# Kernel optimization log

Measured on AMD Instinct MI355X. Metric: run time of the kernel, lower is better.

The kernel has to match this reference:

```python
import jax, jax.numpy as jnp
import numpy as np

N, E, F_IN, F_EDGE, HID, OUT = 100000, 1600000, 128, 8, 128, 2
BN_EPS = 1e-5


def setup_inputs() -> dict:
    key = jax.random.key(0)
    ks = jax.random.split(key, 16)
    rn = lambda k, shape, s=0.05: jax.random.normal(k, shape, jnp.float32) * s
    return {
        "x": jax.random.normal(ks[0], (N, F_IN), jnp.float32),
        "edge_attr": jax.random.uniform(ks[1], (E, F_EDGE), dtype=jnp.float32),
        "edge_index": jax.random.randint(ks[2], (2, E), 0, N, jnp.int32),
        # edge MLP: Linear(F_EDGE, HID) -> ReLU -> Linear(HID, 1) -> Sigmoid
        "ew1_w": rn(ks[3], (F_EDGE, HID)), "ew1_b": jnp.zeros((HID,), jnp.float32),
        "ew2_w": rn(ks[4], (HID, 1)), "ew2_b": jnp.zeros((1,), jnp.float32),
        # SAGEConv layers: lin_l (on aggregated neighbors, with bias) + lin_r (root)
        "w1_l": rn(ks[5], (F_IN, HID)), "b1_l": jnp.zeros((HID,), jnp.float32), "w1_r": rn(ks[6], (F_IN, HID)),
        "w2_l": rn(ks[7], (HID, HID)), "b2_l": jnp.zeros((HID,), jnp.float32), "w2_r": rn(ks[8], (HID, HID)),
        "w3_l": rn(ks[9], (HID, OUT)), "b3_l": jnp.zeros((OUT,), jnp.float32), "w3_r": rn(ks[10], (HID, OUT)),
        # BatchNorm1d (eval mode: running stats)
        "bn1_g": jnp.ones((HID,), jnp.float32), "bn1_b": jnp.zeros((HID,), jnp.float32),
        "bn1_m": rn(ks[11], (HID,), 0.01), "bn1_v": jnp.ones((HID,), jnp.float32),
        "bn2_g": jnp.ones((HID,), jnp.float32), "bn2_b": jnp.zeros((HID,), jnp.float32),
        "bn2_m": rn(ks[12], (HID,), 0.01), "bn2_v": jnp.ones((HID,), jnp.float32),
    }


def _sage(x, src, dst, ew, w_l, b_l, w_r):
    # PyG SAGEConv(aggr='mean'): msg = x[src] * edge_weight, mean over incoming edges at dst
    msg = x[src] * ew[:, None]                                  # [E, F]
    s = jax.ops.segment_sum(msg, dst, num_segments=N)           # [N, F]
    deg = jax.ops.segment_sum(jnp.ones((src.shape[0],), x.dtype), dst, num_segments=N)
    agg = s / jnp.maximum(deg, 1.0)[:, None]
    return agg @ w_l + b_l + x @ w_r


def _bn_eval(h, g, b, m, v):
    return (h - m) * jax.lax.rsqrt(v + BN_EPS) * g + b


def reference(x, edge_attr, edge_index,
              ew1_w, ew1_b, ew2_w, ew2_b,
              w1_l, b1_l, w1_r, w2_l, b2_l, w2_r, w3_l, b3_l, w3_r,
              bn1_g, bn1_b, bn1_m, bn1_v, bn2_g, bn2_b, bn2_m, bn2_v):
    src, dst = edge_index[0], edge_index[1]
    # per-edge scalar weight from small MLP
    ew = jax.nn.sigmoid(jax.nn.relu(edge_attr @ ew1_w + ew1_b) @ ew2_w + ew2_b).reshape(-1)
    h = _sage(x, src, dst, ew, w1_l, b1_l, w1_r)
    h = jax.nn.relu(_bn_eval(h, bn1_g, bn1_b, bn1_m, bn1_v))    # dropout no-op in eval
    h = _sage(h, src, dst, ew, w2_l, b2_l, w2_r)
    h = jax.nn.relu(_bn_eval(h, bn2_g, bn2_b, bn2_m, bn2_v))
    return _sage(h, src, dst, ew, w3_l, b3_l, w3_r)
```

## Files before the change

kernel.cpp:

```cpp
#include <hip/hip_runtime.h>
#include <math.h>

#define N_NODES 100000
#define N_EDGES 1600000
#define F_INF   128
#define HIDF    128

typedef __attribute__((ext_vector_type(8)))  short short8;
typedef __attribute__((ext_vector_type(16))) float floatx16;

__device__ __forceinline__ unsigned short f2bf(float f) {
    unsigned u = __float_as_uint(f);
    return (unsigned short)((u + 0x7FFFu + ((u >> 16) & 1u)) >> 16);
}

__global__ __launch_bounds__(256) void k_edge_mlp(
        const float* __restrict__ ea,
        const float* __restrict__ w1, const float* __restrict__ b1,
        const float* __restrict__ w2, const float* __restrict__ b2,
        float* __restrict__ ew) {
    const int lane = threadIdx.x & 63;
    const int cl   = lane & 31;
    const int half = lane >> 5;
    const int wid  = blockIdx.x * (blockDim.x >> 6) + (threadIdx.x >> 6);
    const int nw   = gridDim.x * (blockDim.x >> 6);

    short8 bw[4];
    float  w2c[4];
#pragma unroll
    for (int cb = 0; cb < 4; ++cb) {
        const int n = cb * 32 + cl;
        short8 b;
        if (half == 0) {
#pragma unroll
            for (int j = 0; j < 8; ++j) b[j] = (short)f2bf(w1[j * 128 + n]);
        } else {
            b[0] = (short)f2bf(b1[n]);
#pragma unroll
            for (int j = 1; j < 8; ++j) b[j] = 0;
        }
        bw[cb] = b;
        w2c[cb] = w2[n];
    }
    short8 Abias;
    Abias[0] = (short)0x3F80;
#pragma unroll
    for (int j = 1; j < 8; ++j) Abias[j] = 0;

    floatx16 czero;
#pragma unroll
    for (int r = 0; r < 16; ++r) czero[r] = 0.f;

    const float bias2 = b2[0];

    for (int e0 = wid * 32; e0 < N_EDGES; e0 += nw * 32) {
        short8 Ah;
        if (half == 0) {
            const float4 a0 = *(const float4*)(ea + (size_t)(e0 + cl) * 8);
            const float4 a1 = *(const float4*)(ea + (size_t)(e0 + cl) * 8 + 4);
            Ah[0] = (short)f2bf(a0.x); Ah[1] = (short)f2bf(a0.y);
            Ah[2] = (short)f2bf(a0.z); Ah[3] = (short)f2bf(a0.w);
            Ah[4] = (short)f2bf(a1.x); Ah[5] = (short)f2bf(a1.y);
            Ah[6] = (short)f2bf(a1.z); Ah[7] = (short)f2bf(a1.w);
        } else {
            Ah = Abias;
        }

        float z[16];
#pragma unroll
        for (int r = 0; r < 16; ++r) z[r] = 0.f;

#pragma unroll
        for (int cb = 0; cb < 4; ++cb) {
            floatx16 acc = __builtin_amdgcn_mfma_f32_32x32x16_bf16(Ah, bw[cb], czero, 0, 0, 0);
#pragma unroll
            for (int r = 0; r < 16; ++r)
                z[r] = fmaf(fmaxf(acc[r], 0.f), w2c[cb], z[r]);
        }

#pragma unroll
        for (int m = 1; m <= 16; m <<= 1) {
#pragma unroll
            for (int r = 0; r < 16; ++r) z[r] += __shfl_xor(z[r], m, 64);
        }

        float zz = z[0];
#pragma unroll
        for (int r = 1; r < 16; ++r) zz = (cl == r) ? z[r] : zz;
        if (cl < 16) {
            const int row = (cl & 3) + 8 * (cl >> 2) + 4 * half;
            ew[e0 + row] = 1.f / (1.f + __expf(-(zz + bias2)));
        }
    }
}

__global__ void k_deg(const int* __restrict__ dst, int* __restrict__ deg,
                      unsigned char* __restrict__ rank) {
    int e = blockIdx.x * 256 + threadIdx.x;
    if (e < N_EDGES) rank[e] = (unsigned char)atomicAdd(&deg[dst[e]], 1);
}

__global__ void k_scan1(const int* __restrict__ deg, int* __restrict__ incl,
                        int* __restrict__ bsum) {
    __shared__ int sm[1024];
    const int tid = threadIdx.x;
    const int gi  = blockIdx.x * 1024 + tid;
    int v = (gi < N_NODES) ? deg[gi] : 0;
    sm[tid] = v;
    __syncthreads();
    for (int off = 1; off < 1024; off <<= 1) {
        int t = (tid >= off) ? sm[tid - off] : 0;
        __syncthreads();
        sm[tid] += t;
        __syncthreads();
    }
    if (gi < N_NODES) incl[gi] = sm[tid];
    if (tid == 1023) bsum[blockIdx.x] = sm[1023];
}

__global__ void k_scan2(const int* __restrict__ bsum, int* __restrict__ boff, int nb) {
    __shared__ int sm[128];
    const int tid = threadIdx.x;
    int v = (tid < nb) ? bsum[tid] : 0;
    sm[tid] = v;
    __syncthreads();
    for (int off = 1; off < 128; off <<= 1) {
        int t = (tid >= off) ? sm[tid - off] : 0;
        __syncthreads();
        sm[tid] += t;
        __syncthreads();
    }
    boff[tid] = sm[tid] - v;
}

__global__ void k_scan3(const int* __restrict__ incl, const int* __restrict__ boff,
                        int* __restrict__ rowptr) {
    int i = blockIdx.x * 256 + threadIdx.x;
    if (i < N_NODES) rowptr[i + 1] = boff[i >> 10] + incl[i];
    if (i == 0) rowptr[0] = 0;
}

__global__ void k_fill(const int* __restrict__ src, const int* __restrict__ dst,
                       const float* __restrict__ ew, const int* __restrict__ rowptr,
                       const unsigned char* __restrict__ rank,
                       unsigned* __restrict__ cw) {
    int e = blockIdx.x * 256 + threadIdx.x;
    if (e < N_EDGES) {
        int d   = dst[e];
        int pos = rowptr[d] + (int)rank[e];
        unsigned wb = (unsigned)f2bf(ew[e]) & 0x7FFFu;
        cw[pos] = ((unsigned)src[e] << 15) | wb;
    }
}

__global__ void k_cast(const float* __restrict__ x, unsigned short* __restrict__ xb) {
    const int i = (blockIdx.x * 256 + threadIdx.x) * 4;
    const float4 v = *(const float4*)(x + i);
    ushort4 o;
    o.x = f2bf(v.x); o.y = f2bf(v.y); o.z = f2bf(v.z); o.w = f2bf(v.w);
    *(ushort4*)(xb + i) = o;
}

__global__ __launch_bounds__(256) void k_agg16(
        const unsigned short* __restrict__ xb, const int* __restrict__ rowptr,
        const unsigned* __restrict__ cw, float* __restrict__ aggout) {
    const int lane = threadIdx.x & 63;
    const int half = lane >> 5;
    const int cl   = lane & 31;
    const int node = blockIdx.x * (blockDim.x >> 6) + (threadIdx.x >> 6);
    if (node >= N_NODES) return;
    const int s = rowptr[node], e = rowptr[node + 1];
    float a0 = 0.f, a1 = 0.f, a2 = 0.f, a3 = 0.f;

    for (int j0 = s; j0 < e; j0 += 8) {
        int ss[4]; float ww[4];
#pragma unroll
        for (int u = 0; u < 4; ++u) {
            const int j  = j0 + 2 * u + half;
            const int jc = min(j, e - 1);
            const unsigned p = cw[jc];
            ss[u] = (int)(p >> 15);
            ww[u] = (j < e) ? __uint_as_float((p & 0x7FFFu) << 16) : 0.f;
        }
        uint2 g[4];
#pragma unroll
        for (int u = 0; u < 4; ++u)
            g[u] = *(const uint2*)(xb + (size_t)ss[u] * 128 + cl * 4);
#pragma unroll
        for (int u = 0; u < 4; ++u) {
            const float f0 = __uint_as_float(g[u].x << 16);
            const float f1 = __uint_as_float(g[u].x & 0xFFFF0000u);
            const float f2 = __uint_as_float(g[u].y << 16);
            const float f3 = __uint_as_float(g[u].y & 0xFFFF0000u);
            a0 = fmaf(ww[u], f0, a0);
            a1 = fmaf(ww[u], f1, a1);
            a2 = fmaf(ww[u], f2, a2);
            a3 = fmaf(ww[u], f3, a3);
        }
    }
    a0 += __shfl_xor(a0, 32, 64);
    a1 += __shfl_xor(a1, 32, 64);
    a2 += __shfl_xor(a2, 32, 64);
    a3 += __shfl_xor(a3, 32, 64);
    if (half == 0) {
        const float inv = 1.f / fmaxf((float)(e - s), 1.f);
        float4 r;
        r.x = a0 * inv; r.y = a1 * inv; r.z = a2 * inv; r.w = a3 * inv;
        *(float4*)(aggout + (size_t)node * 128 + cl * 4) = r;
    }
}

__global__ void k_wpack(const float* __restrict__ Wl, const float* __restrict__ Wr,
                        short* __restrict__ Whi, short* __restrict__ Wlo) {
    int idx = blockIdx.x * 256 + threadIdx.x;
    int j  = idx & 7;
    int L  = (idx >> 3) & 63;
    int cb = (idx >> 9) & 3;
    int kb = (idx >> 11);
    int k  = kb * 16 + (L >> 5) * 8 + j;
    int n  = cb * 32 + (L & 31);
    float a = (k < 128) ? Wl[k * 128 + n] : Wr[(k - 128) * 128 + n];
    unsigned short hb = f2bf(a);
    float hf = __uint_as_float((unsigned)hb << 16);
    Whi[idx] = (short)hb;
    Wlo[idx] = (short)f2bf(a - hf);
}

__global__ __launch_bounds__(256) void k_gemm_mfma(
    const float* __restrict__ Aagg, const float* __restrict__ Ax,
    const short* __restrict__ Whi, const short* __restrict__ Wlo,
    const float* __restrict__ bl,
    const float* __restrict__ bng, const float* __restrict__ bnb,
    const float* __restrict__ bnm, const float* __restrict__ bnv,
    float* __restrict__ out, unsigned short* __restrict__ out16) {
    const int tid  = threadIdx.x;
    const int lane = tid & 63;
    const int w    = tid >> 6;
    const int row0 = blockIdx.x * 128 + w * 32;
    const int rrow = lane & 31;
    const int kq   = lane >> 5;
    const int arow = min(row0 + rrow, N_NODES - 1);

    floatx16 acc[4];
#pragma unroll
    for (int cb = 0; cb < 4; ++cb)
#pragma unroll
        for (int r = 0; r < 16; ++r) acc[cb][r] = 0.f;

    const float* Abase0 = Aagg + (size_t)arow * 128 + kq * 8;
    const float* Abase1 = Ax   + (size_t)arow * 128 + kq * 8;

#pragma unroll 2
    for (int kb = 0; kb < 16; ++kb) {
        const float* ap = ((kb < 8) ? Abase0 : Abase1) + (kb & 7) * 16;
        const float4 a0 = *(const float4*)(ap);
        const float4 a1 = *(const float4*)(ap + 4);
        const float av[8] = {a0.x, a0.y, a0.z, a0.w, a1.x, a1.y, a1.z, a1.w};
        short8 Ah, Al;
#pragma unroll
        for (int j = 0; j < 8; ++j) {
            unsigned short hb = f2bf(av[j]);
            float hf = __uint_as_float((unsigned)hb << 16);
            Ah[j] = (short)hb;
            Al[j] = (short)f2bf(av[j] - hf);
        }
#pragma unroll
        for (int cb = 0; cb < 4; ++cb) {
            const size_t wo = ((size_t)(kb * 4 + cb) * 64 + lane) * 8;
            const short8 wh = *(const short8*)(Whi + wo);
            const short8 wl = *(const short8*)(Wlo + wo);
            acc[cb] = __builtin_amdgcn_mfma_f32_32x32x16_bf16(Ah, wh, acc[cb], 0, 0, 0);
            acc[cb] = __builtin_amdgcn_mfma_f32_32x32x16_bf16(Al, wh, acc[cb], 0, 0, 0);
            acc[cb] = __builtin_amdgcn_mfma_f32_32x32x16_bf16(Ah, wl, acc[cb], 0, 0, 0);
        }
    }

#pragma unroll
    for (int cb = 0; cb < 4; ++cb) {
        const int c = cb * 32 + (lane & 31);
        const float s = bng[c] * rsqrtf(bnv[c] + 1e-5f);
        const float t = (bl[c] - bnm[c]) * s + bnb[c];
#pragma unroll
        for (int r = 0; r < 16; ++r) {
            const int row = row0 + (r & 3) + 8 * (r >> 2) + 4 * kq;
            if (row < N_NODES) {
                const float v = fmaxf(fmaf(acc[cb][r], s, t), 0.f);
                out[(size_t)row * 128 + c] = v;
                if (out16) out16[(size_t)row * 128 + c] = f2bf(v);
            }
        }
    }
}

__global__ void k_lin3(const float* __restrict__ h, const float* __restrict__ w3l,
                       const float* __restrict__ w3r, float* __restrict__ t4) {
    const int lane = threadIdx.x & 63;
    const int node = blockIdx.x * (blockDim.x >> 6) + (threadIdx.x >> 6);
    if (node >= N_NODES) return;
    float h0 = h[(size_t)node * 128 + lane];
    float h1 = h[(size_t)node * 128 + 64 + lane];
    float2 wl0 = *(const float2*)(w3l + lane * 2);
    float2 wl1 = *(const float2*)(w3l + (64 + lane) * 2);
    float2 wr0 = *(const float2*)(w3r + lane * 2);
    float2 wr1 = *(const float2*)(w3r + (64 + lane) * 2);
    float p0 = h0 * wl0.x + h1 * wl1.x;
    float p1 = h0 * wl0.y + h1 * wl1.y;
    float p2 = h0 * wr0.x + h1 * wr1.x;
    float p3 = h0 * wr0.y + h1 * wr1.y;
#pragma unroll
    for (int m = 1; m < 64; m <<= 1) {
        p0 += __shfl_xor(p0, m, 64);
        p1 += __shfl_xor(p1, m, 64);
        p2 += __shfl_xor(p2, m, 64);
        p3 += __shfl_xor(p3, m, 64);
    }
    if (lane == 0) {
        float4 o; o.x = p0; o.y = p1; o.z = p2; o.w = p3;
        *(float4*)(t4 + (size_t)node * 4) = o;
    }
}

__global__ void k_out(const float* __restrict__ t4, const int* __restrict__ rowptr,
                      const unsigned* __restrict__ cw,
                      const float* __restrict__ b3, float* __restrict__ out) {
    const int lane = threadIdx.x & 63;
    const int node = blockIdx.x * (blockDim.x >> 6) + (threadIdx.x >> 6);
    if (node >= N_NODES) return;
    const int s = rowptr[node], e = rowptr[node + 1];
    float a0 = 0.f, a1 = 0.f;
    for (int j = s + lane; j < e; j += 64) {
        const unsigned p = cw[j];
        const int   sr = (int)(p >> 15);
        const float w  = __uint_as_float((p & 0x7FFFu) << 16);
        float2 t = *(const float2*)(t4 + (size_t)sr * 4);
        a0 += w * t.x; a1 += w * t.y;
    }
#pragma unroll
    for (int m = 1; m < 64; m <<= 1) {
        a0 += __shfl_xor(a0, m, 64);
        a1 += __shfl_xor(a1, m, 64);
    }
    if (lane == 0) {
        float inv = 1.f / fmaxf((float)(e - s), 1.f);
        float2 o;
        o.x = a0 * inv + b3[0] + t4[(size_t)node * 4 + 2];
        o.y = a1 * inv + b3[1] + t4[(size_t)node * 4 + 3];
        *(float2*)(out + (size_t)node * 2) = o;
    }
}

extern "C" void kernel_launch(void* const* d_in, const int* in_sizes, int n_in,
                              void* d_out, int out_size, void* d_ws, size_t ws_size,
                              hipStream_t stream) {
    const float* x    = (const float*)d_in[0];
    const float* ea   = (const float*)d_in[1];
    const int*   ei   = (const int*)d_in[2];
    const float* ew1w = (const float*)d_in[3];
    const float* ew1b = (const float*)d_in[4];
    const float* ew2w = (const float*)d_in[5];
    const float* ew2b = (const float*)d_in[6];
    const float* w1l  = (const float*)d_in[7];
    const float* b1l  = (const float*)d_in[8];
    const float* w1r  = (const float*)d_in[9];
    const float* w2l  = (const float*)d_in[10];
    const float* b2l  = (const float*)d_in[11];
    const float* w2r  = (const float*)d_in[12];
    const float* w3l  = (const float*)d_in[13];
    const float* b3l  = (const float*)d_in[14];
    const float* w3r  = (const float*)d_in[15];
    const float* bn1g = (const float*)d_in[16];
    const float* bn1b = (const float*)d_in[17];
    const float* bn1m = (const float*)d_in[18];
    const float* bn1v = (const float*)d_in[19];
    const float* bn2g = (const float*)d_in[20];
    const float* bn2b = (const float*)d_in[21];
    const float* bn2m = (const float*)d_in[22];
    const float* bn2v = (const float*)d_in[23];

    const int* src = ei;
    const int* dst = ei + N_EDGES;
    float* out = (float*)d_out;

    size_t off = 0;
    auto carve = [&](size_t bytes) -> void* {
        void* p = (char*)d_ws + off;
        off += (bytes + 255) & ~(size_t)255;
        return p;
    };
    float* ew     = (float*)carve((size_t)N_EDGES * 4);
    unsigned* cw  = (unsigned*)carve((size_t)N_EDGES * 4);
    unsigned char* rank = (unsigned char*)carve((size_t)N_EDGES);
    int*   rowptr = (int*)carve((size_t)(N_NODES + 1) * 4);
    int*   deg    = (int*)carve((size_t)N_NODES * 4);
    int*   bsum   = (int*)carve(128 * 4);
    int*   boff   = (int*)carve(128 * 4);
    int*   incl   = (int*)carve((size_t)N_NODES * 4);
    float* agg    = (float*)carve((size_t)N_NODES * 128 * 4);
    float* hA     = (float*)carve((size_t)N_NODES * 128 * 4);
    float* hB     = (float*)carve((size_t)N_NODES * 128 * 4);
    float* t4     = (float*)carve((size_t)N_NODES * 4 * 4);
    short* W1hi   = (short*)carve(32768 * 2);
    short* W1lo   = (short*)carve(32768 * 2);
    short* W2hi   = (short*)carve(32768 * 2);
    short* W2lo   = (short*)carve(32768 * 2);
    unsigned short* xb   = (unsigned short*)carve((size_t)N_NODES * 128 * 2);
    unsigned short* hA16 = (unsigned short*)carve((size_t)N_NODES * 128 * 2);
    (void)ws_size; (void)n_in; (void)in_sizes; (void)out_size;

    hipMemsetAsync(deg, 0, (size_t)N_NODES * 4, stream);

    const int EB = (N_EDGES + 255) / 256;
    const int NB_SCAN = (N_NODES + 1023) / 1024;
    const int NWB = (N_NODES + 3) / 4;
    const int GB = (N_NODES + 127) / 128;
    const int CB = (N_NODES * 128 / 4 + 255) / 256;

    k_deg<<<EB, 256, 0, stream>>>(dst, deg, rank);
    k_cast<<<CB, 256, 0, stream>>>(x, xb);
    k_edge_mlp<<<2048, 256, 0, stream>>>(ea, ew1w, ew1b, ew2w, ew2b, ew);
    k_wpack<<<128, 256, 0, stream>>>(w1l, w1r, W1hi, W1lo);
    k_wpack<<<128, 256, 0, stream>>>(w2l, w2r, W2hi, W2lo);
    k_scan1<<<NB_SCAN, 1024, 0, stream>>>(deg, incl, bsum);
    k_scan2<<<1, 128, 0, stream>>>(bsum, boff, NB_SCAN);
    k_scan3<<<(N_NODES + 255) / 256, 256, 0, stream>>>(incl, boff, rowptr);
    k_fill<<<EB, 256, 0, stream>>>(src, dst, ew, rowptr, rank, cw);

    k_agg16<<<NWB, 256, 0, stream>>>(xb, rowptr, cw, agg);
    k_gemm_mfma<<<GB, 256, 0, stream>>>(agg, x, W1hi, W1lo, b1l,
                                        bn1g, bn1b, bn1m, bn1v, hA, hA16);
    k_agg16<<<NWB, 256, 0, stream>>>(hA16, rowptr, cw, agg);
    k_gemm_mfma<<<GB, 256, 0, stream>>>(agg, hA, W2hi, W2lo, b2l,
                                        bn2g, bn2b, bn2m, bn2v, hB, nullptr);
    k_lin3<<<NWB, 256, 0, stream>>>(hB, w3l, w3r, t4);
    k_out<<<NWB, 256, 0, stream>>>(t4, rowptr, cw, b3l, out);
}
```

Baseline: 591.5 us.

## Fuse neighbor aggregation with MFMA GEMM and layer-3 projection per 32-node tile

```diff
diff --git a/kernel.cpp b/kernel.cpp
--- a/kernel.cpp
+++ b/kernel.cpp
@@ -12,6 +12,9 @@
 __device__ __forceinline__ unsigned short f2bf(float f) {
     unsigned u = __float_as_uint(f);
     return (unsigned short)((u + 0x7FFFu + ((u >> 16) & 1u)) >> 16);
+}
+__device__ __forceinline__ float bf2f(unsigned short h) {
+    return __uint_as_float((unsigned)h << 16);
 }
 
 __global__ __launch_bounds__(256) void k_edge_mlp(
@@ -94,10 +97,19 @@
     }
 }
 
-__global__ void k_deg(const int* __restrict__ dst, int* __restrict__ deg,
-                      unsigned char* __restrict__ rank) {
-    int e = blockIdx.x * 256 + threadIdx.x;
-    if (e < N_EDGES) rank[e] = (unsigned char)atomicAdd(&deg[dst[e]], 1);
+__global__ void k_cast_deg(const float* __restrict__ x, unsigned short* __restrict__ xb,
+                           const int* __restrict__ dst, int* __restrict__ deg,
+                           unsigned char* __restrict__ rank) {
+    const int gid = blockIdx.x * 256 + threadIdx.x;
+    const int i = gid * 4;
+    const float4 v = *(const float4*)(x + i);
+    ushort4 o;
+    o.x = f2bf(v.x); o.y = f2bf(v.y); o.z = f2bf(v.z); o.w = f2bf(v.w);
+    *(ushort4*)(xb + i) = o;
+    if ((gid & 1) == 0) {
+        const int e = gid >> 1;
+        rank[e] = (unsigned char)atomicAdd(&deg[dst[e]], 1);
+    }
 }
 
 __global__ void k_scan1(const int* __restrict__ deg, int* __restrict__ incl,
@@ -150,63 +162,6 @@
         int pos = rowptr[d] + (int)rank[e];
         unsigned wb = (unsigned)f2bf(ew[e]) & 0x7FFFu;
         cw[pos] = ((unsigned)src[e] << 15) | wb;
-    }
-}
-
-__global__ void k_cast(const float* __restrict__ x, unsigned short* __restrict__ xb) {
-    const int i = (blockIdx.x * 256 + threadIdx.x) * 4;
-    const float4 v = *(const float4*)(x + i);
-    ushort4 o;
-    o.x = f2bf(v.x); o.y = f2bf(v.y); o.z = f2bf(v.z); o.w = f2bf(v.w);
-    *(ushort4*)(xb + i) = o;
-}
-
-__global__ __launch_bounds__(256) void k_agg16(
-        const unsigned short* __restrict__ xb, const int* __restrict__ rowptr,
-        const unsigned* __restrict__ cw, float* __restrict__ aggout) {
-    const int lane = threadIdx.x & 63;
-    const int half = lane >> 5;
-    const int cl   = lane & 31;
-    const int node = blockIdx.x * (blockDim.x >> 6) + (threadIdx.x >> 6);
-    if (node >= N_NODES) return;
-    const int s = rowptr[node], e = rowptr[node + 1];
-    float a0 = 0.f, a1 = 0.f, a2 = 0.f, a3 = 0.f;
-
-    for (int j0 = s; j0 < e; j0 += 8) {
-        int ss[4]; float ww[4];
-#pragma unroll
-        for (int u = 0; u < 4; ++u) {
-            const int j  = j0 + 2 * u + half;
-            const int jc = min(j, e - 1);
-            const unsigned p = cw[jc];
-            ss[u] = (int)(p >> 15);
-            ww[u] = (j < e) ? __uint_as_float((p & 0x7FFFu) << 16) : 0.f;
-        }
-        uint2 g[4];
-#pragma unroll
-        for (int u = 0; u < 4; ++u)
-            g[u] = *(const uint2*)(xb + (size_t)ss[u] * 128 + cl * 4);
-#pragma unroll
-        for (int u = 0; u < 4; ++u) {
-            const float f0 = __uint_as_float(g[u].x << 16);
-            const float f1 = __uint_as_float(g[u].x & 0xFFFF0000u);
-            const float f2 = __uint_as_float(g[u].y << 16);
-            const float f3 = __uint_as_float(g[u].y & 0xFFFF0000u);
-            a0 = fmaf(ww[u], f0, a0);
-            a1 = fmaf(ww[u], f1, a1);
-            a2 = fmaf(ww[u], f2, a2);
-            a3 = fmaf(ww[u], f3, a3);
-        }
-    }
-    a0 += __shfl_xor(a0, 32, 64);
-    a1 += __shfl_xor(a1, 32, 64);
-    a2 += __shfl_xor(a2, 32, 64);
-    a3 += __shfl_xor(a3, 32, 64);
-    if (half == 0) {
-        const float inv = 1.f / fmaxf((float)(e - s), 1.f);
-        float4 r;
-        r.x = a0 * inv; r.y = a1 * inv; r.z = a2 * inv; r.w = a3 * inv;
-        *(float4*)(aggout + (size_t)node * 128 + cl * 4) = r;
     }
 }
 
@@ -226,44 +181,92 @@
     Wlo[idx] = (short)f2bf(a - hf);
 }
 
-__global__ __launch_bounds__(256) void k_gemm_mfma(
-    const float* __restrict__ Aagg, const float* __restrict__ Ax,
-    const short* __restrict__ Whi, const short* __restrict__ Wlo,
-    const float* __restrict__ bl,
-    const float* __restrict__ bng, const float* __restrict__ bnb,
-    const float* __restrict__ bnm, const float* __restrict__ bnv,
-    float* __restrict__ out, unsigned short* __restrict__ out16) {
-    const int tid  = threadIdx.x;
-    const int lane = tid & 63;
-    const int w    = tid >> 6;
-    const int row0 = blockIdx.x * 128 + w * 32;
-    const int rrow = lane & 31;
-    const int kq   = lane >> 5;
-    const int arow = min(row0 + rrow, N_NODES - 1);
-
+__global__ __launch_bounds__(64, 2) void k_fused1(
+        const unsigned short* __restrict__ xb, const int* __restrict__ rowptr,
+        const unsigned* __restrict__ cw, const float* __restrict__ Ax,
+        const short* __restrict__ Whi, const short* __restrict__ Wlo,
+        const float* __restrict__ bl,
+        const float* __restrict__ bng, const float* __restrict__ bnb,
+        const float* __restrict__ bnm, const float* __restrict__ bnv,
+        unsigned short* __restrict__ outHi, unsigned short* __restrict__ outLo) {
+    __shared__ unsigned short HiS[32 * 128];
+    __shared__ unsigned short LoS[32 * 128];
+    const int lane = threadIdx.x & 63;
+    const int half = lane >> 5;
+    const int cl   = lane & 31;
+    const int row0 = blockIdx.x * 32;
+
+    unsigned short* const myLds = half ? LoS : HiS;
+
+#pragma unroll 1
+    for (int nl = 0; nl < 32; ++nl) {
+        const int node = row0 + nl;
+        float a0 = 0.f, a1 = 0.f, a2 = 0.f, a3 = 0.f;
+        {
+            const int s = rowptr[node], e = rowptr[node + 1];
+            for (int j0 = s; j0 < e; j0 += 8) {
+                int ss[4]; float ww[4];
+#pragma unroll
+                for (int u = 0; u < 4; ++u) {
+                    const int j  = j0 + 2 * u + half;
+                    const int jc = min(j, e - 1);
+                    const unsigned p = cw[jc];
+                    ss[u] = (int)(p >> 15);
+                    ww[u] = (j < e) ? __uint_as_float((p & 0x7FFFu) << 16) : 0.f;
+                }
+                uint2 g[4];
+#pragma unroll
+                for (int u = 0; u < 4; ++u)
+                    g[u] = *(const uint2*)(xb + (size_t)ss[u] * 128 + cl * 4);
+#pragma unroll
+                for (int u = 0; u < 4; ++u) {
+                    const float f0 = __uint_as_float(g[u].x << 16);
+                    const float f1 = __uint_as_float(g[u].x & 0xFFFF0000u);
+                    const float f2 = __uint_as_float(g[u].y << 16);
+                    const float f3 = __uint_as_float(g[u].y & 0xFFFF0000u);
+                    a0 = fmaf(ww[u], f0, a0);
+                    a1 = fmaf(ww[u], f1, a1);
+                    a2 = fmaf(ww[u], f2, a2);
+                    a3 = fmaf(ww[u], f3, a3);
+                }
+            }
+            a0 += __shfl_xor(a0, 32, 64);
+            a1 += __shfl_xor(a1, 32, 64);
+            a2 += __shfl_xor(a2, 32, 64);
+            a3 += __shfl_xor(a3, 32, 64);
+            const float inv = 1.f / fmaxf((float)(e - s), 1.f);
+            a0 *= inv; a1 *= inv; a2 *= inv; a3 *= inv;
+        }
+        unsigned short v0, v1, v2, v3;
+        if (half == 0) {
+            v0 = f2bf(a0); v1 = f2bf(a1); v2 = f2bf(a2); v3 = f2bf(a3);
+        } else {
+            const unsigned short h0 = f2bf(a0), h1 = f2bf(a1),
+                                 h2 = f2bf(a2), h3 = f2bf(a3);
+            v0 = f2bf(a0 - bf2f(h0)); v1 = f2bf(a1 - bf2f(h1));
+            v2 = f2bf(a2 - bf2f(h2)); v3 = f2bf(a3 - bf2f(h3));
+        }
+        uint2 wv;
+        wv.x = (unsigned)v0 | ((unsigned)v1 << 16);
+        wv.y = (unsigned)v2 | ((unsigned)v3 << 16);
+        const int slot = (cl >> 1) ^ (nl & 15);
+        *(uint2*)(myLds + nl * 128 + slot * 8 + (cl & 1) * 4) = wv;
+    }
+
+    const int rrow = cl;
+    const int kq   = half;
+    const int arow = row0 + rrow;
     floatx16 acc[4];
 #pragma unroll
     for (int cb = 0; cb < 4; ++cb)
 #pragma unroll
         for (int r = 0; r < 16; ++r) acc[cb][r] = 0.f;
 
-    const float* Abase0 = Aagg + (size_t)arow * 128 + kq * 8;
-    const float* Abase1 = Ax   + (size_t)arow * 128 + kq * 8;
-
 #pragma unroll 2
-    for (int kb = 0; kb < 16; ++kb) {
-        const float* ap = ((kb < 8) ? Abase0 : Abase1) + (kb & 7) * 16;
-        const float4 a0 = *(const float4*)(ap);
-        const float4 a1 = *(const float4*)(ap + 4);
-        const float av[8] = {a0.x, a0.y, a0.z, a0.w, a1.x, a1.y, a1.z, a1.w};
-        short8 Ah, Al;
-#pragma unroll
-        for (int j = 0; j < 8; ++j) {
-            unsigned short hb = f2bf(av[j]);
-            float hf = __uint_as_float((unsigned)hb << 16);
-            Ah[j] = (short)hb;
-            Al[j] = (short)f2bf(av[j] - hf);
-        }
+    for (int kb = 0; kb < 8; ++kb) {
+        const int slot = (2 * kb + kq) ^ (rrow & 15);
+        const short8 Ah = *(const short8*)(HiS + rrow * 128 + slot * 8);
+        const short8 Al = *(const short8*)(LoS + rrow * 128 + slot * 8);
 #pragma unroll
         for (int cb = 0; cb < 4; ++cb) {
             const size_t wo = ((size_t)(kb * 4 + cb) * 64 + lane) * 8;
@@ -275,48 +278,199 @@
         }
     }
 
+    const float* Abase1 = Ax + (size_t)arow * 128 + kq * 8;
+#pragma unroll 2
+    for (int kb = 8; kb < 16; ++kb) {
+        const float* ap = Abase1 + (kb & 7) * 16;
+        const float4 p0 = *(const float4*)(ap);
+        const float4 p1 = *(const float4*)(ap + 4);
+        const float av[8] = {p0.x, p0.y, p0.z, p0.w, p1.x, p1.y, p1.z, p1.w};
+        short8 Ah, Al;
+#pragma unroll
+        for (int j = 0; j < 8; ++j) {
+            const unsigned short hb = f2bf(av[j]);
+            Ah[j] = (short)hb;
+            Al[j] = (short)f2bf(av[j] - bf2f(hb));
+        }
+#pragma unroll
+        for (int cb = 0; cb < 4; ++cb) {
+            const size_t wo = ((size_t)(kb * 4 + cb) * 64 + lane) * 8;
+            const short8 wh = *(const short8*)(Whi + wo);
+            const short8 wl = *(const short8*)(Wlo + wo);
+            acc[cb] = __builtin_amdgcn_mfma_f32_32x32x16_bf16(Ah, wh, acc[cb], 0, 0, 0);
+            acc[cb] = __builtin_amdgcn_mfma_f32_32x32x16_bf16(Al, wh, acc[cb], 0, 0, 0);
+            acc[cb] = __builtin_amdgcn_mfma_f32_32x32x16_bf16(Ah, wl, acc[cb], 0, 0, 0);
+        }
+    }
+
 #pragma unroll
     for (int cb = 0; cb < 4; ++cb) {
-        const int c = cb * 32 + (lane & 31);
+        const int c = cb * 32 + cl;
         const float s = bng[c] * rsqrtf(bnv[c] + 1e-5f);
         const float t = (bl[c] - bnm[c]) * s + bnb[c];
 #pragma unroll
         for (int r = 0; r < 16; ++r) {
             const int row = row0 + (r & 3) + 8 * (r >> 2) + 4 * kq;
-            if (row < N_NODES) {
-                const float v = fmaxf(fmaf(acc[cb][r], s, t), 0.f);
-                out[(size_t)row * 128 + c] = v;
-                if (out16) out16[(size_t)row * 128 + c] = f2bf(v);
+            const float v = fmaxf(fmaf(acc[cb][r], s, t), 0.f);
+            const unsigned short hb = f2bf(v);
+            outHi[(size_t)row * 128 + c] = hb;
+            outLo[(size_t)row * 128 + c] = f2bf(v - bf2f(hb));
+        }
+    }
+}
+
+__global__ __launch_bounds__(64, 2) void k_fused2(
+        const unsigned short* __restrict__ hHi, const unsigned short* __restrict__ hLo,
+        const int* __restrict__ rowptr, const unsigned* __restrict__ cw,
+        const short* __restrict__ Whi, const short* __restrict__ Wlo,
+        const float* __restrict__ bl,
+        const float* __restrict__ bng, const float* __restrict__ bnb,
+        const float* __restrict__ bnm, const float* __restrict__ bnv,
+        const float* __restrict__ w3l, const float* __restrict__ w3r,
+        float* __restrict__ t4) {
+    __shared__ unsigned short HiS[32 * 128];
+    __shared__ unsigned short LoS[32 * 128];
+    const int lane = threadIdx.x & 63;
+    const int half = lane >> 5;
+    const int cl   = lane & 31;
+    const int row0 = blockIdx.x * 32;
+
+    unsigned short* const myLds = half ? LoS : HiS;
+
+#pragma unroll 1
+    for (int nl = 0; nl < 32; ++nl) {
+        const int node = row0 + nl;
+        float a0 = 0.f, a1 = 0.f, a2 = 0.f, a3 = 0.f;
+        {
+            const int s = rowptr[node], e = rowptr[node + 1];
+            for (int j0 = s; j0 < e; j0 += 8) {
+                int ss[4]; float ww[4];
+#pragma unroll
+                for (int u = 0; u < 4; ++u) {
+                    const int j  = j0 + 2 * u + half;
+                    const int jc = min(j, e - 1);
+                    const unsigned p = cw[jc];
+                    ss[u] = (int)(p >> 15);
+                    ww[u] = (j < e) ? __uint_as_float((p & 0x7FFFu) << 16) : 0.f;
+                }
+                uint2 g[4];
+#pragma unroll
+                for (int u = 0; u < 4; ++u)
+                    g[u] = *(const uint2*)(hHi + (size_t)ss[u] * 128 + cl * 4);
+#pragma unroll
+                for (int u = 0; u < 4; ++u) {
+                    const float f0 = __uint_as_float(g[u].x << 16);
+                    const float f1 = __uint_as_float(g[u].x & 0xFFFF0000u);
+                    const float f2 = __uint_as_float(g[u].y << 16);
+                    const float f3 = __uint_as_float(g[u].y & 0xFFFF0000u);
+                    a0 = fmaf(ww[u], f0, a0);
+                    a1 = fmaf(ww[u], f1, a1);
+                    a2 = fmaf(ww[u], f2, a2);
+                    a3 = fmaf(ww[u], f3, a3);
+                }
             }
-        }
-    }
-}
-
-__global__ void k_lin3(const float* __restrict__ h, const float* __restrict__ w3l,
-                       const float* __restrict__ w3r, float* __restrict__ t4) {
-    const int lane = threadIdx.x & 63;
-    const int node = blockIdx.x * (blockDim.x >> 6) + (threadIdx.x >> 6);
-    if (node >= N_NODES) return;
-    float h0 = h[(size_t)node * 128 + lane];
-    float h1 = h[(size_t)node * 128 + 64 + lane];
-    float2 wl0 = *(const float2*)(w3l + lane * 2);
-    float2 wl1 = *(const float2*)(w3l + (64 + lane) * 2);
-    float2 wr0 = *(const float2*)(w3r + lane * 2);
-    float2 wr1 = *(const float2*)(w3r + (64 + lane) * 2);
-    float p0 = h0 * wl0.x + h1 * wl1.x;
-    float p1 = h0 * wl0.y + h1 * wl1.y;
-    float p2 = h0 * wr0.x + h1 * wr1.x;
-    float p3 = h0 * wr0.y + h1 * wr1.y;
-#pragma unroll
-    for (int m = 1; m < 64; m <<= 1) {
-        p0 += __shfl_xor(p0, m, 64);
-        p1 += __shfl_xor(p1, m, 64);
-        p2 += __shfl_xor(p2, m, 64);
-        p3 += __shfl_xor(p3, m, 64);
-    }
-    if (lane == 0) {
-        float4 o; o.x = p0; o.y = p1; o.z = p2; o.w = p3;
-        *(float4*)(t4 + (size_t)node * 4) = o;
+            a0 += __shfl_xor(a0, 32, 64);
+            a1 += __shfl_xor(a1, 32, 64);
+            a2 += __shfl_xor(a2, 32, 64);
+            a3 += __shfl_xor(a3, 32, 64);
+            const float inv = 1.f / fmaxf((float)(e - s), 1.f);
+            a0 *= inv; a1 *= inv; a2 *= inv; a3 *= inv;
+        }
+        unsigned short v0, v1, v2, v3;
+        if (half == 0) {
+            v0 = f2bf(a0); v1 = f2bf(a1); v2 = f2bf(a2); v3 = f2bf(a3);
+        } else {
+            const unsigned short h0 = f2bf(a0), h1 = f2bf(a1),
+                                 h2 = f2bf(a2), h3 = f2bf(a3);
+            v0 = f2bf(a0 - bf2f(h0)); v1 = f2bf(a1 - bf2f(h1));
+            v2 = f2bf(a2 - bf2f(h2)); v3 = f2bf(a3 - bf2f(h3));
+        }
+        uint2 wv;
+        wv.x = (unsigned)v0 | ((unsigned)v1 << 16);
+        wv.y = (unsigned)v2 | ((unsigned)v3 << 16);
+        const int slot = (cl >> 1) ^ (nl & 15);
+        *(uint2*)(myLds + nl * 128 + slot * 8 + (cl & 1) * 4) = wv;
+    }
+
+    const int rrow = cl;
+    const int kq   = half;
+    const int arow = row0 + rrow;
+    floatx16 acc[4];
+#pragma unroll
+    for (int cb = 0; cb < 4; ++cb)
+#pragma unroll
+        for (int r = 0; r < 16; ++r) acc[cb][r] = 0.f;
+
+#pragma unroll 2
+    for (int kb = 0; kb < 8; ++kb) {
+        const int slot = (2 * kb + kq) ^ (rrow & 15);
+        const short8 Ah = *(const short8*)(HiS + rrow * 128 + slot * 8);
+        const short8 Al = *(const short8*)(LoS + rrow * 128 + slot * 8);
+#pragma unroll
+        for (int cb = 0; cb < 4; ++cb) {
+            const size_t wo = ((size_t)(kb * 4 + cb) * 64 + lane) * 8;
+            const short8 wh = *(const short8*)(Whi + wo);
+            const short8 wl = *(const short8*)(Wlo + wo);
+            acc[cb] = __builtin_amdgcn_mfma_f32_32x32x16_bf16(Ah, wh, acc[cb], 0, 0, 0);
+            acc[cb] = __builtin_amdgcn_mfma_f32_32x32x16_bf16(Al, wh, acc[cb], 0, 0, 0);
+            acc[cb] = __builtin_amdgcn_mfma_f32_32x32x16_bf16(Ah, wl, acc[cb], 0, 0, 0);
+        }
+    }
+
+#pragma unroll 2
+    for (int kb = 8; kb < 16; ++kb) {
+        const size_t axo = (size_t)arow * 128 + (kb & 7) * 16 + kq * 8;
+        const short8 Ah = *(const short8*)(hHi + axo);
+        const short8 Al = *(const short8*)(hLo + axo);
+#pragma unroll
+        for (int cb = 0; cb < 4; ++cb) {
+            const size_t wo = ((size_t)(kb * 4 + cb) * 64 + lane) * 8;
+            const short8 wh = *(const short8*)(Whi + wo);
+            const short8 wl = *(const short8*)(Wlo + wo);
+            acc[cb] = __builtin_amdgcn_mfma_f32_32x32x16_bf16(Ah, wh, acc[cb], 0, 0, 0);
+            acc[cb] = __builtin_amdgcn_mfma_f32_32x32x16_bf16(Al, wh, acc[cb], 0, 0, 0);
+            acc[cb] = __builtin_amdgcn_mfma_f32_32x32x16_bf16(Ah, wl, acc[cb], 0, 0, 0);
+        }
+    }
+
+    float q0[16], q1[16], q2[16], q3[16];
+#pragma unroll
+    for (int r = 0; r < 16; ++r) { q0[r] = 0.f; q1[r] = 0.f; q2[r] = 0.f; q3[r] = 0.f; }
+#pragma unroll
+    for (int cb = 0; cb < 4; ++cb) {
+        const int c = cb * 32 + cl;
+        const float s = bng[c] * rsqrtf(bnv[c] + 1e-5f);
+        const float t = (bl[c] - bnm[c]) * s + bnb[c];
+        const float2 wL = *(const float2*)(w3l + c * 2);
+        const float2 wR = *(const float2*)(w3r + c * 2);
+#pragma unroll
+        for (int r = 0; r < 16; ++r) {
+            const float v = fmaxf(fmaf(acc[cb][r], s, t), 0.f);
+            q0[r] = fmaf(v, wL.x, q0[r]);
+            q1[r] = fmaf(v, wL.y, q1[r]);
+            q2[r] = fmaf(v, wR.x, q2[r]);
+            q3[r] = fmaf(v, wR.y, q3[r]);
+        }
+    }
+#pragma unroll
+    for (int m = 1; m <= 16; m <<= 1) {
+#pragma unroll
+        for (int r = 0; r < 16; ++r) {
+            q0[r] += __shfl_xor(q0[r], m, 64);
+            q1[r] += __shfl_xor(q1[r], m, 64);
+            q2[r] += __shfl_xor(q2[r], m, 64);
+            q3[r] += __shfl_xor(q3[r], m, 64);
+        }
+    }
+    float z0 = q0[0], z1 = q1[0], z2 = q2[0], z3 = q3[0];
+#pragma unroll
+    for (int r = 1; r < 16; ++r) {
+        if (cl == r) { z0 = q0[r]; z1 = q1[r]; z2 = q2[r]; z3 = q3[r]; }
+    }
+    if (cl < 16) {
+        const int row = row0 + (cl & 3) + 8 * (cl >> 2) + 4 * kq;
+        float4 o; o.x = z0; o.y = z1; o.z = z2; o.w = z3;
+        *(float4*)(t4 + (size_t)row * 4) = o;
     }
 }
 
@@ -395,16 +549,14 @@
     int*   bsum   = (int*)carve(128 * 4);
     int*   boff   = (int*)carve(128 * 4);
     int*   incl   = (int*)carve((size_t)N_NODES * 4);
-    float* agg    = (float*)carve((size_t)N_NODES * 128 * 4);
-    float* hA     = (float*)carve((size_t)N_NODES * 128 * 4);
-    float* hB     = (float*)carve((size_t)N_NODES * 128 * 4);
     float* t4     = (float*)carve((size_t)N_NODES * 4 * 4);
     short* W1hi   = (short*)carve(32768 * 2);
     short* W1lo   = (short*)carve(32768 * 2);
     short* W2hi   = (short*)carve(32768 * 2);
     short* W2lo   = (short*)carve(32768 * 2);
-    unsigned short* xb   = (unsigned short*)carve((size_t)N_NODES * 128 * 2);
-    unsigned short* hA16 = (unsigned short*)carve((size_t)N_NODES * 128 * 2);
+    unsigned short* xb  = (unsigned short*)carve((size_t)N_NODES * 128 * 2);
+    unsigned short* hHi = (unsigned short*)carve((size_t)N_NODES * 128 * 2);
+    unsigned short* hLo = (unsigned short*)carve((size_t)N_NODES * 128 * 2);
     (void)ws_size; (void)n_in; (void)in_sizes; (void)out_size;
 
     hipMemsetAsync(deg, 0, (size_t)N_NODES * 4, stream);
@@ -412,11 +564,10 @@
     const int EB = (N_EDGES + 255) / 256;
     const int NB_SCAN = (N_NODES + 1023) / 1024;
     const int NWB = (N_NODES + 3) / 4;
-    const int GB = (N_NODES + 127) / 128;
     const int CB = (N_NODES * 128 / 4 + 255) / 256;
-
-    k_deg<<<EB, 256, 0, stream>>>(dst, deg, rank);
-    k_cast<<<CB, 256, 0, stream>>>(x, xb);
+    const int FB = N_NODES / 32;
+
+    k_cast_deg<<<CB, 256, 0, stream>>>(x, xb, dst, deg, rank);
     k_edge_mlp<<<2048, 256, 0, stream>>>(ea, ew1w, ew1b, ew2w, ew2b, ew);
     k_wpack<<<128, 256, 0, stream>>>(w1l, w1r, W1hi, W1lo);
     k_wpack<<<128, 256, 0, stream>>>(w2l, w2r, W2hi, W2lo);
@@ -425,12 +576,9 @@
     k_scan3<<<(N_NODES + 255) / 256, 256, 0, stream>>>(incl, boff, rowptr);
     k_fill<<<EB, 256, 0, stream>>>(src, dst, ew, rowptr, rank, cw);
 
-    k_agg16<<<NWB, 256, 0, stream>>>(xb, rowptr, cw, agg);
-    k_gemm_mfma<<<GB, 256, 0, stream>>>(agg, x, W1hi, W1lo, b1l,
-                                        bn1g, bn1b, bn1m, bn1v, hA, hA16);
-    k_agg16<<<NWB, 256, 0, stream>>>(hA16, rowptr, cw, agg);
-    k_gemm_mfma<<<GB, 256, 0, stream>>>(agg, hA, W2hi, W2lo, b2l,
-                                        bn2g, bn2b, bn2m, bn2v, hB, nullptr);
-    k_lin3<<<NWB, 256, 0, stream>>>(hB, w3l, w3r, t4);
+    k_fused1<<<FB, 64, 0, stream>>>(xb, rowptr, cw, x, W1hi, W1lo, b1l,
+                                    bn1g, bn1b, bn1m, bn1v, hHi, hLo);
+    k_fused2<<<FB, 64, 0, stream>>>(hHi, hLo, rowptr, cw, W2hi, W2lo, b2l,
+                                    bn2g, bn2b, bn2m, bn2v, w3l, w3r, t4);
     k_out<<<NWB, 256, 0, stream>>>(t4, rowptr, cw, b3l, out);
 }
```

After: 659.6 us. 1.12x slower.

## Store activations as bf16 hi/lo pairs, fuse lin3 into gemm2 and deg into cast

Applied to the files above, without the earlier changes.

```diff
diff --git a/kernel.cpp b/kernel.cpp
--- a/kernel.cpp
+++ b/kernel.cpp
@@ -12,6 +12,9 @@
 __device__ __forceinline__ unsigned short f2bf(float f) {
     unsigned u = __float_as_uint(f);
     return (unsigned short)((u + 0x7FFFu + ((u >> 16) & 1u)) >> 16);
+}
+__device__ __forceinline__ float bf2f(unsigned short h) {
+    return __uint_as_float((unsigned)h << 16);
 }
 
 __global__ __launch_bounds__(256) void k_edge_mlp(
@@ -94,10 +97,25 @@
     }
 }
 
-__global__ void k_deg(const int* __restrict__ dst, int* __restrict__ deg,
-                      unsigned char* __restrict__ rank) {
-    int e = blockIdx.x * 256 + threadIdx.x;
-    if (e < N_EDGES) rank[e] = (unsigned char)atomicAdd(&deg[dst[e]], 1);
+__global__ void k_cast_deg(const float* __restrict__ x,
+                           unsigned short* __restrict__ xbHi,
+                           unsigned short* __restrict__ xbLo,
+                           const int* __restrict__ dst, int* __restrict__ deg,
+                           unsigned char* __restrict__ rank) {
+    const int gid = blockIdx.x * 256 + threadIdx.x;
+    const int i = gid * 4;
+    const float4 v = *(const float4*)(x + i);
+    ushort4 h, l;
+    h.x = f2bf(v.x); l.x = f2bf(v.x - bf2f(h.x));
+    h.y = f2bf(v.y); l.y = f2bf(v.y - bf2f(h.y));
+    h.z = f2bf(v.z); l.z = f2bf(v.z - bf2f(h.z));
+    h.w = f2bf(v.w); l.w = f2bf(v.w - bf2f(h.w));
+    *(ushort4*)(xbHi + i) = h;
+    *(ushort4*)(xbLo + i) = l;
+    if ((gid & 1) == 0) {
+        const int e = gid >> 1;
+        rank[e] = (unsigned char)atomicAdd(&deg[dst[e]], 1);
+    }
 }
 
 __global__ void k_scan1(const int* __restrict__ deg, int* __restrict__ incl,
@@ -150,63 +168,6 @@
         int pos = rowptr[d] + (int)rank[e];
         unsigned wb = (unsigned)f2bf(ew[e]) & 0x7FFFu;
         cw[pos] = ((unsigned)src[e] << 15) | wb;
-    }
-}
-
-__global__ void k_cast(const float* __restrict__ x, unsigned short* __restrict__ xb) {
-    const int i = (blockIdx.x * 256 + threadIdx.x) * 4;
-    const float4 v = *(const float4*)(x + i);
-    ushort4 o;
-    o.x = f2bf(v.x); o.y = f2bf(v.y); o.z = f2bf(v.z); o.w = f2bf(v.w);
-    *(ushort4*)(xb + i) = o;
-}
-
-__global__ __launch_bounds__(256) void k_agg16(
-        const unsigned short* __restrict__ xb, const int* __restrict__ rowptr,
-        const unsigned* __restrict__ cw, float* __restrict__ aggout) {
-    const int lane = threadIdx.x & 63;
-    const int half = lane >> 5;
-    const int cl   = lane & 31;
-    const int node = blockIdx.x * (blockDim.x >> 6) + (threadIdx.x >> 6);
-    if (node >= N_NODES) return;
-    const int s = rowptr[node], e = rowptr[node + 1];
-    float a0 = 0.f, a1 = 0.f, a2 = 0.f, a3 = 0.f;
-
-    for (int j0 = s; j0 < e; j0 += 8) {
-        int ss[4]; float ww[4];
-#pragma unroll
-        for (int u = 0; u < 4; ++u) {
-            const int j  = j0 + 2 * u + half;
-            const int jc = min(j, e - 1);
-            const unsigned p = cw[jc];
-            ss[u] = (int)(p >> 15);
-            ww[u] = (j < e) ? __uint_as_float((p & 0x7FFFu) << 16) : 0.f;
-        }
-        uint2 g[4];
-#pragma unroll
-        for (int u = 0; u < 4; ++u)
-            g[u] = *(const uint2*)(xb + (size_t)ss[u] * 128 + cl * 4);
-#pragma unroll
-        for (int u = 0; u < 4; ++u) {
-            const float f0 = __uint_as_float(g[u].x << 16);
-            const float f1 = __uint_as_float(g[u].x & 0xFFFF0000u);
-            const float f2 = __uint_as_float(g[u].y << 16);
-            const float f3 = __uint_as_float(g[u].y & 0xFFFF0000u);
-            a0 = fmaf(ww[u], f0, a0);
-            a1 = fmaf(ww[u], f1, a1);
-            a2 = fmaf(ww[u], f2, a2);
-            a3 = fmaf(ww[u], f3, a3);
-        }
-    }
-    a0 += __shfl_xor(a0, 32, 64);
-    a1 += __shfl_xor(a1, 32, 64);
-    a2 += __shfl_xor(a2, 32, 64);
-    a3 += __shfl_xor(a3, 32, 64);
-    if (half == 0) {
-        const float inv = 1.f / fmaxf((float)(e - s), 1.f);
-        float4 r;
-        r.x = a0 * inv; r.y = a1 * inv; r.z = a2 * inv; r.w = a3 * inv;
-        *(float4*)(aggout + (size_t)node * 128 + cl * 4) = r;
     }
 }
 
@@ -226,13 +187,69 @@
     Wlo[idx] = (short)f2bf(a - hf);
 }
 
-__global__ __launch_bounds__(256) void k_gemm_mfma(
-    const float* __restrict__ Aagg, const float* __restrict__ Ax,
+__global__ __launch_bounds__(256) void k_agg16(
+        const unsigned short* __restrict__ xb, const int* __restrict__ rowptr,
+        const unsigned* __restrict__ cw,
+        unsigned short* __restrict__ aggHi, unsigned short* __restrict__ aggLo) {
+    const int lane = threadIdx.x & 63;
+    const int half = lane >> 5;
+    const int cl   = lane & 31;
+    const int node = blockIdx.x * (blockDim.x >> 6) + (threadIdx.x >> 6);
+    if (node >= N_NODES) return;
+    const int s = rowptr[node], e = rowptr[node + 1];
+    float a0 = 0.f, a1 = 0.f, a2 = 0.f, a3 = 0.f;
+
+    for (int j0 = s; j0 < e; j0 += 8) {
+        int ss[4]; float ww[4];
+#pragma unroll
+        for (int u = 0; u < 4; ++u) {
+            const int j  = j0 + 2 * u + half;
+            const int jc = min(j, e - 1);
+            const unsigned p = cw[jc];
+            ss[u] = (int)(p >> 15);
+            ww[u] = (j < e) ? __uint_as_float((p & 0x7FFFu) << 16) : 0.f;
+        }
+        uint2 g[4];
+#pragma unroll
+        for (int u = 0; u < 4; ++u)
+            g[u] = *(const uint2*)(xb + (size_t)ss[u] * 128 + cl * 4);
+#pragma unroll
+        for (int u = 0; u < 4; ++u) {
+            const float f0 = __uint_as_float(g[u].x << 16);
+            const float f1 = __uint_as_float(g[u].x & 0xFFFF0000u);
+            const float f2 = __uint_as_float(g[u].y << 16);
+            const float f3 = __uint_as_float(g[u].y & 0xFFFF0000u);
+            a0 = fmaf(ww[u], f0, a0);
+            a1 = fmaf(ww[u], f1, a1);
+            a2 = fmaf(ww[u], f2, a2);
+            a3 = fmaf(ww[u], f3, a3);
+        }
+    }
+    a0 += __shfl_xor(a0, 32, 64);
+    a1 += __shfl_xor(a1, 32, 64);
+    a2 += __shfl_xor(a2, 32, 64);
+    a3 += __shfl_xor(a3, 32, 64);
+    if (half == 0) {
+        const float inv = 1.f / fmaxf((float)(e - s), 1.f);
+        a0 *= inv; a1 *= inv; a2 *= inv; a3 *= inv;
+        ushort4 h, l;
+        h.x = f2bf(a0); l.x = f2bf(a0 - bf2f(h.x));
+        h.y = f2bf(a1); l.y = f2bf(a1 - bf2f(h.y));
+        h.z = f2bf(a2); l.z = f2bf(a2 - bf2f(h.z));
+        h.w = f2bf(a3); l.w = f2bf(a3 - bf2f(h.w));
+        *(ushort4*)(aggHi + (size_t)node * 128 + cl * 4) = h;
+        *(ushort4*)(aggLo + (size_t)node * 128 + cl * 4) = l;
+    }
+}
+
+__global__ __launch_bounds__(256) void k_gemm1(
+    const unsigned short* __restrict__ AaggHi, const unsigned short* __restrict__ AaggLo,
+    const unsigned short* __restrict__ AxHi, const unsigned short* __restrict__ AxLo,
     const short* __restrict__ Whi, const short* __restrict__ Wlo,
     const float* __restrict__ bl,
     const float* __restrict__ bng, const float* __restrict__ bnb,
     const float* __restrict__ bnm, const float* __restrict__ bnv,
-    float* __restrict__ out, unsigned short* __restrict__ out16) {
+    unsigned short* __restrict__ outHi, unsigned short* __restrict__ outLo) {
     const int tid  = threadIdx.x;
     const int lane = tid & 63;
     const int w    = tid >> 6;
@@ -247,23 +264,13 @@
 #pragma unroll
         for (int r = 0; r < 16; ++r) acc[cb][r] = 0.f;
 
-    const float* Abase0 = Aagg + (size_t)arow * 128 + kq * 8;
-    const float* Abase1 = Ax   + (size_t)arow * 128 + kq * 8;
+    const size_t abase = (size_t)arow * 128 + kq * 8;
 
 #pragma unroll 2
     for (int kb = 0; kb < 16; ++kb) {
-        const float* ap = ((kb < 8) ? Abase0 : Abase1) + (kb & 7) * 16;
-        const float4 a0 = *(const float4*)(ap);
-        const float4 a1 = *(const float4*)(ap + 4);
-        const float av[8] = {a0.x, a0.y, a0.z, a0.w, a1.x, a1.y, a1.z, a1.w};
-        short8 Ah, Al;
-#pragma unroll
-        for (int j = 0; j < 8; ++j) {
-            unsigned short hb = f2bf(av[j]);
-            float hf = __uint_as_float((unsigned)hb << 16);
-            Ah[j] = (short)hb;
-            Al[j] = (short)f2bf(av[j] - hf);
-        }
+        const size_t ao = abase + (kb & 7) * 16;
+        const short8 Ah = *(const short8*)(((kb < 8) ? AaggHi : AxHi) + ao);
+        const short8 Al = *(const short8*)(((kb < 8) ? AaggLo : AxLo) + ao);
 #pragma unroll
         for (int cb = 0; cb < 4; ++cb) {
             const size_t wo = ((size_t)(kb * 4 + cb) * 64 + lane) * 8;
@@ -285,38 +292,96 @@
             const int row = row0 + (r & 3) + 8 * (r >> 2) + 4 * kq;
             if (row < N_NODES) {
                 const float v = fmaxf(fmaf(acc[cb][r], s, t), 0.f);
-                out[(size_t)row * 128 + c] = v;
-                if (out16) out16[(size_t)row * 128 + c] = f2bf(v);
+                const unsigned short hb = f2bf(v);
+                outHi[(size_t)row * 128 + c] = hb;
+                outLo[(size_t)row * 128 + c] = f2bf(v - bf2f(hb));
             }
         }
     }
 }
 
-__global__ void k_lin3(const float* __restrict__ h, const float* __restrict__ w3l,
-                       const float* __restrict__ w3r, float* __restrict__ t4) {
-    const int lane = threadIdx.x & 63;
-    const int node = blockIdx.x * (blockDim.x >> 6) + (threadIdx.x >> 6);
-    if (node >= N_NODES) return;
-    float h0 = h[(size_t)node * 128 + lane];
-    float h1 = h[(size_t)node * 128 + 64 + lane];
-    float2 wl0 = *(const float2*)(w3l + lane * 2);
-    float2 wl1 = *(const float2*)(w3l + (64 + lane) * 2);
-    float2 wr0 = *(const float2*)(w3r + lane * 2);
-    float2 wr1 = *(const float2*)(w3r + (64 + lane) * 2);
-    float p0 = h0 * wl0.x + h1 * wl1.x;
-    float p1 = h0 * wl0.y + h1 * wl1.y;
-    float p2 = h0 * wr0.x + h1 * wr1.x;
-    float p3 = h0 * wr0.y + h1 * wr1.y;
-#pragma unroll
-    for (int m = 1; m < 64; m <<= 1) {
-        p0 += __shfl_xor(p0, m, 64);
-        p1 += __shfl_xor(p1, m, 64);
-        p2 += __shfl_xor(p2, m, 64);
-        p3 += __shfl_xor(p3, m, 64);
-    }
-    if (lane == 0) {
-        float4 o; o.x = p0; o.y = p1; o.z = p2; o.w = p3;
-        *(float4*)(t4 + (size_t)node * 4) = o;
+__global__ __launch_bounds__(256) void k_gemm2(
+    const unsigned short* __restrict__ AaggHi, const unsigned short* __restrict__ AaggLo,
+    const unsigned short* __restrict__ AxHi, const unsigned short* __restrict__ AxLo,
+    const short* __restrict__ Whi, const short* __restrict__ Wlo,
+    const float* __restrict__ bl,
+    const float* __restrict__ bng, const float* __restrict__ bnb,
+    const float* __restrict__ bnm, const float* __restrict__ bnv,
+    const float* __restrict__ w3l, const float* __restrict__ w3r,
+    float* __restrict__ t4) {
+    const int tid  = threadIdx.x;
+    const int lane = tid & 63;
+    const int w    = tid >> 6;
+    const int row0 = blockIdx.x * 128 + w * 32;
+    const int rrow = lane & 31;
+    const int kq   = lane >> 5;
+    const int arow = min(row0 + rrow, N_NODES - 1);
+    const int cl   = lane & 31;
+
+    floatx16 acc[4];
+#pragma unroll
+    for (int cb = 0; cb < 4; ++cb)
+#pragma unroll
+        for (int r = 0; r < 16; ++r) acc[cb][r] = 0.f;
+
+    const size_t abase = (size_t)arow * 128 + kq * 8;
+
+#pragma unroll 2
+    for (int kb = 0; kb < 16; ++kb) {
+        const size_t ao = abase + (kb & 7) * 16;
+        const short8 Ah = *(const short8*)(((kb < 8) ? AaggHi : AxHi) + ao);
+        const short8 Al = *(const short8*)(((kb < 8) ? AaggLo : AxLo) + ao);
+#pragma unroll
+        for (int cb = 0; cb < 4; ++cb) {
+            const size_t wo = ((size_t)(kb * 4 + cb) * 64 + lane) * 8;
+            const short8 wh = *(const short8*)(Whi + wo);
+            const short8 wl = *(const short8*)(Wlo + wo);
+            acc[cb] = __builtin_amdgcn_mfma_f32_32x32x16_bf16(Ah, wh, acc[cb], 0, 0, 0);
+            acc[cb] = __builtin_amdgcn_mfma_f32_32x32x16_bf16(Al, wh, acc[cb], 0, 0, 0);
+            acc[cb] = __builtin_amdgcn_mfma_f32_32x32x16_bf16(Ah, wl, acc[cb], 0, 0, 0);
+        }
+    }
+
+    float q0[16], q1[16], q2[16], q3[16];
+#pragma unroll
+    for (int r = 0; r < 16; ++r) { q0[r] = 0.f; q1[r] = 0.f; q2[r] = 0.f; q3[r] = 0.f; }
+#pragma unroll
+    for (int cb = 0; cb < 4; ++cb) {
+        const int c = cb * 32 + cl;
+        const float s = bng[c] * rsqrtf(bnv[c] + 1e-5f);
+        const float t = (bl[c] - bnm[c]) * s + bnb[c];
+        const float2 wL = *(const float2*)(w3l + c * 2);
+        const float2 wR = *(const float2*)(w3r + c * 2);
+#pragma unroll
+        for (int r = 0; r < 16; ++r) {
+            const float v = fmaxf(fmaf(acc[cb][r], s, t), 0.f);
+            q0[r] = fmaf(v, wL.x, q0[r]);
+            q1[r] = fmaf(v, wL.y, q1[r]);
+            q2[r] = fmaf(v, wR.x, q2[r]);
+            q3[r] = fmaf(v, wR.y, q3[r]);
+        }
+    }
+#pragma unroll
+    for (int m = 1; m <= 16; m <<= 1) {
+#pragma unroll
+        for (int r = 0; r < 16; ++r) {
+            q0[r] += __shfl_xor(q0[r], m, 64);
+            q1[r] += __shfl_xor(q1[r], m, 64);
+            q2[r] += __shfl_xor(q2[r], m, 64);
+            q3[r] += __shfl_xor(q3[r], m, 64);
+        }
+    }
+    float z0 = q0[0], z1 = q1[0], z2 = q2[0], z3 = q3[0];
+#pragma unroll
+    for (int r = 1; r < 16; ++r) {
+        if (cl == r) { z0 = q0[r]; z1 = q1[r]; z2 = q2[r]; z3 = q3[r]; }
+    }
+    if (cl < 16) {
+        const int row = row0 + (cl & 3) + 8 * (cl >> 2) + 4 * kq;
+        if (row < N_NODES) {
+            float4 o; o.x = z0; o.y = z1; o.z = z2; o.w = z3;
+            *(float4*)(t4 + (size_t)row * 4) = o;
+        }
     }
 }
 
@@ -395,16 +460,17 @@
     int*   bsum   = (int*)carve(128 * 4);
     int*   boff   = (int*)carve(128 * 4);
     int*   incl   = (int*)carve((size_t)N_NODES * 4);
-    float* agg    = (float*)carve((size_t)N_NODES * 128 * 4);
-    float* hA     = (float*)carve((size_t)N_NODES * 128 * 4);
-    float* hB     = (float*)carve((size_t)N_NODES * 128 * 4);
     float* t4     = (float*)carve((size_t)N_NODES * 4 * 4);
     short* W1hi   = (short*)carve(32768 * 2);
     short* W1lo   = (short*)carve(32768 * 2);
     short* W2hi   = (short*)carve(32768 * 2);
     short* W2lo   = (short*)carve(32768 * 2);
-    unsigned short* xb   = (unsigned short*)carve((size_t)N_NODES * 128 * 2);
-    unsigned short* hA16 = (unsigned short*)carve((size_t)N_NODES * 128 * 2);
+    unsigned short* xbHi  = (unsigned short*)carve((size_t)N_NODES * 128 * 2);
+    unsigned short* xbLo  = (unsigned short*)carve((size_t)N_NODES * 128 * 2);
+    unsigned short* aggHi = (unsigned short*)carve((size_t)N_NODES * 128 * 2);
+    unsigned short* aggLo = (unsigned short*)carve((size_t)N_NODES * 128 * 2);
+    unsigned short* hHi   = (unsigned short*)carve((size_t)N_NODES * 128 * 2);
+    unsigned short* hLo   = (unsigned short*)carve((size_t)N_NODES * 128 * 2);
     (void)ws_size; (void)n_in; (void)in_sizes; (void)out_size;
 
     hipMemsetAsync(deg, 0, (size_t)N_NODES * 4, stream);
@@ -415,8 +481,7 @@
     const int GB = (N_NODES + 127) / 128;
     const int CB = (N_NODES * 128 / 4 + 255) / 256;
 
-    k_deg<<<EB, 256, 0, stream>>>(dst, deg, rank);
-    k_cast<<<CB, 256, 0, stream>>>(x, xb);
+    k_cast_deg<<<CB, 256, 0, stream>>>(x, xbHi, xbLo, dst, deg, rank);
     k_edge_mlp<<<2048, 256, 0, stream>>>(ea, ew1w, ew1b, ew2w, ew2b, ew);
     k_wpack<<<128, 256, 0, stream>>>(w1l, w1r, W1hi, W1lo);
     k_wpack<<<128, 256, 0, stream>>>(w2l, w2r, W2hi, W2lo);
@@ -425,12 +490,11 @@
     k_scan3<<<(N_NODES + 255) / 256, 256, 0, stream>>>(incl, boff, rowptr);
     k_fill<<<EB, 256, 0, stream>>>(src, dst, ew, rowptr, rank, cw);
 
-    k_agg16<<<NWB, 256, 0, stream>>>(xb, rowptr, cw, agg);
-    k_gemm_mfma<<<GB, 256, 0, stream>>>(agg, x, W1hi, W1lo, b1l,
-                                        bn1g, bn1b, bn1m, bn1v, hA, hA16);
-    k_agg16<<<NWB, 256, 0, stream>>>(hA16, rowptr, cw, agg);
-    k_gemm_mfma<<<GB, 256, 0, stream>>>(agg, hA, W2hi, W2lo, b2l,
-                                        bn2g, bn2b, bn2m, bn2v, hB, nullptr);
-    k_lin3<<<NWB, 256, 0, stream>>>(hB, w3l, w3r, t4);
+    k_agg16<<<NWB, 256, 0, stream>>>(xbHi, rowptr, cw, aggHi, aggLo);
+    k_gemm1<<<GB, 256, 0, stream>>>(aggHi, aggLo, xbHi, xbLo, W1hi, W1lo, b1l,
+                                    bn1g, bn1b, bn1m, bn1v, hHi, hLo);
+    k_agg16<<<NWB, 256, 0, stream>>>(hHi, rowptr, cw, aggHi, aggLo);
+    k_gemm2<<<GB, 256, 0, stream>>>(aggHi, aggLo, hHi, hLo, W2hi, W2lo, b2l,
+                                    bn2g, bn2b, bn2m, bn2v, w3l, w3r, t4);
     k_out<<<NWB, 256, 0, stream>>>(t4, rowptr, cw, b3l, out);
 }
```

Result: no change. 594.3 us (+0.5%).
